# Kernel tuning notes

Measured on AMD Instinct MI355X. Metric: run time of the kernel, lower is better.

Reference implementation:

```python
import jax, jax.numpy as jnp
import numpy as np

L, HID, NH, DH, OUT = 20, 512, 8, 64, 1000
NPAT, PS = 14, 16
IN_DIM = 3 * PS * PS          # 768
SEQ = NPAT * NPAT + 1         # 197
BATCH = 64
EPS = 1e-5


def _pos_embeddings(seq_len, d):
    # sin(i/10000^(j/d)) for even j, cos(i/10000^((j-1)/d)) for odd j
    i = jnp.arange(seq_len, dtype=jnp.float32)[:, None]
    j = jnp.arange(d)
    je = (j - (j % 2)).astype(jnp.float32)
    ang = i / jnp.power(10000.0, je / d)
    return jnp.where(j % 2 == 0, jnp.sin(ang), jnp.cos(ang))


def _layernorm(x, g, b):
    m = jnp.mean(x, axis=-1, keepdims=True)
    v = jnp.mean(jnp.square(x - m), axis=-1, keepdims=True)
    return (x - m) * jax.lax.rsqrt(v + EPS) * g + b


def setup_inputs() -> dict:
    key = jax.random.key(0)
    ks = jax.random.split(key, 12)
    r = lambda k, sh: jax.random.normal(k, sh, dtype=jnp.float32) * 0.02
    return {
        "x": jax.random.normal(ks[0], (BATCH, 3, 224, 224), dtype=jnp.float32),
        "embed_W": r(ks[1], (IN_DIM, HID)),
        "embed_b": jnp.zeros((HID,), jnp.float32),
        "cls": r(ks[2], (HID,)),
        "ln1_g": jnp.ones((L, HID), jnp.float32),
        "ln1_b": jnp.zeros((L, HID), jnp.float32),
        "qW": r(ks[3], (L, NH, DH, DH)),
        "qb": jnp.zeros((L, NH, DH), jnp.float32),
        "kW": r(ks[4], (L, NH, DH, DH)),
        "kb": jnp.zeros((L, NH, DH), jnp.float32),
        "vW": r(ks[5], (L, NH, DH, DH)),
        "vb": jnp.zeros((L, NH, DH), jnp.float32),
        "ln2_g": jnp.ones((L, HID), jnp.float32),
        "ln2_b": jnp.zeros((L, HID), jnp.float32),
        "mlp1_W": r(ks[6], (L, HID, 4 * HID)),
        "mlp1_b": jnp.zeros((L, 4 * HID), jnp.float32),
        "mlp2_W": r(ks[7], (L, 4 * HID, HID)),
        "mlp2_b": jnp.zeros((L, HID), jnp.float32),
        "head_W": r(ks[8], (HID, OUT)),
        "head_b": jnp.zeros((OUT,), jnp.float32),
    }


def reference(x, embed_W, embed_b, cls, ln1_g, ln1_b, qW, qb, kW, kb, vW, vb,
              ln2_g, ln2_b, mlp1_W, mlp1_b, mlp2_W, mlp2_b, head_W, head_b):
    n = x.shape[0]
    # patchify: [n,3,224,224] -> [n,196,768], flatten order (c, ph, pw)
    p = x.reshape(n, 3, NPAT, PS, NPAT, PS)
    p = p.transpose(0, 2, 4, 1, 3, 5).reshape(n, NPAT * NPAT, IN_DIM)
    tokens = p @ embed_W + embed_b                      # [n,196,HID]
    cls_tok = jnp.broadcast_to(cls, (n, 1, HID))
    h = jnp.concatenate([cls_tok, tokens], axis=1)      # [n,197,HID]
    h = h + _pos_embeddings(SEQ, HID)

    scale = 1.0 / jnp.sqrt(jnp.float32(DH))

    def step(h, params):
        (g1, b1, qw, qb_, kw, kb_, vw, vb_, g2, b2, w1, b1m, w2, b2m) = params
        y = _layernorm(h, g1, b1)                       # [n,S,HID]
        yh = y.reshape(n, SEQ, NH, DH)
        # torch Linear: out = seq @ W.T + b; qw stored as [NH, out, in]
        q = jnp.einsum('nshd,hed->nshe', yh, qw) + qb_
        k = jnp.einsum('nshd,hed->nshe', yh, kw) + kb_
        v = jnp.einsum('nshd,hed->nshe', yh, vw) + vb_
        att = jax.nn.softmax(jnp.einsum('nqhd,nkhd->nhqk', q, k) * scale, axis=-1)
        o = jnp.einsum('nhqk,nkhd->nqhd', att, v).reshape(n, SEQ, HID)
        h = h + o
        z = _layernorm(h, g2, b2)
        z = jax.nn.gelu(z @ w1 + b1m, approximate=False) @ w2 + b2m
        return h + z, None

    params = (ln1_g, ln1_b, qW, qb, kW, kb, vW, vb,
              ln2_g, ln2_b, mlp1_W, mlp1_b, mlp2_W, mlp2_b)
    h, _ = jax.lax.scan(step, h, params)
    logits = h[:, 0] @ head_W + head_b
    return jax.nn.softmax(logits, axis=-1)
```

## Files before the change

### kernel.cpp

```cpp
#include <hip/hip_runtime.h>
#include <hip/hip_bf16.h>
#include <math.h>

#define LAY 20
#define HID 512
#define NH 8
#define DH 64
#define OUTC 1000
#define SEQ 197
#define SPAD 224
#define BATCH 64
#define TT (BATCH*SEQ)
#define M2 12800
#define NPTOK (BATCH*196)
#define IN_DIM 768

typedef __attribute__((ext_vector_type(8))) short bf16x8;
typedef __attribute__((ext_vector_type(4))) float f32x4;

__device__ __forceinline__ ushort f2bf(float f){
  __hip_bfloat16 h = __float2bfloat16(f);
  return *(ushort*)&h;
}
__device__ __forceinline__ float bf2f(ushort u){
  __hip_bfloat16 h = *(__hip_bfloat16*)&u;
  return __bfloat162float(h);
}

__device__ __forceinline__ float posemb(int i, int j){
  float je = (float)(j & ~1);
  float ang = (float)i * powf(10000.0f, -je * (1.0f/(float)HID));
  return (j & 1) ? cosf(ang) : sinf(ang);
}

__device__ __forceinline__ float gelu_exact(float x){
  return 0.5f * x * (1.0f + erff(x * 0.70710678118654752f));
}

__device__ __forceinline__ void gld_lds16(const ushort* g, ushort* l){
  __builtin_amdgcn_global_load_lds((const __attribute__((address_space(1))) void*)g,
                                   (__attribute__((address_space(3))) void*)l, 16, 0, 0);
}

__global__ __launch_bounds__(512)
void pos_kernel(float* __restrict__ pos){
  int i = blockIdx.x, j = threadIdx.x;
  pos[(size_t)i*HID + j] = posemb(i, j);
}

__global__ __launch_bounds__(256)
void convt_kernel(const float* __restrict__ src, ushort* __restrict__ dst,
                  int R, int C){
  __shared__ float tile[32][33];
  const float* s = src + (size_t)blockIdx.z * R * C;
  ushort* d      = dst + (size_t)blockIdx.z * R * C;
  int r0 = blockIdx.y * 32, c0 = blockIdx.x * 32;
  int tc = threadIdx.x & 31, tr = threadIdx.x >> 5;
  #pragma unroll
  for (int i = 0; i < 4; ++i)
    tile[tr + i*8][tc] = s[(size_t)(r0 + tr + i*8)*C + c0 + tc];
  __syncthreads();
  #pragma unroll
  for (int i = 0; i < 4; ++i)
    d[(size_t)(c0 + tr + i*8)*R + r0 + tc] = f2bf(tile[tc][tr + i*8]);
}

__global__ __launch_bounds__(256)
void cvt_kernel(const float* __restrict__ src, ushort* __restrict__ dst, int count){
  int idx = blockIdx.x * 256 + threadIdx.x;
  if (idx < count) dst[idx] = f2bf(src[idx]);
}

__global__ __launch_bounds__(256)
void patchify_kernel(const float* __restrict__ x, ushort* __restrict__ p){
  int idx = blockIdx.x * 256 + threadIdx.x;
  int r   = idx / 768, cdx = idx - r * 768;
  int n   = r / 196,  pp  = r - n * 196;
  int pr  = pp / 14,  pc  = pp - pr * 14;
  int c   = cdx >> 8, rem = cdx & 255;
  int ph  = rem >> 4, pw  = rem & 15;
  p[idx] = f2bf(x[ (((size_t)(n*3 + c)*224) + pr*16 + ph)*224 + pc*16 + pw ]);
}

__global__ __launch_bounds__(512)
void cls_kernel(const float* __restrict__ cls, const float* __restrict__ pos,
                float* __restrict__ h){
  int n = blockIdx.x, e = threadIdx.x;
  h[(size_t)n*SEQ*HID + e] = cls[e] + pos[e];
}

template<int BN, int EPI>
__global__ __launch_bounds__(256, 4)
void gemm_pipe(const ushort* __restrict__ A, const ushort* __restrict__ Bt,
               const float* __restrict__ bias, void* __restrict__ Cv,
               int K, int N, int Mreal, int NBX, const float* __restrict__ pos){
  constexpr int BM = 128;
  constexpr int MF = 4, NF = BN/32;
  constexpr int BQ = BN/64;
  constexpr int TBS = 8192 + BN*64;
  constexpr int ES = NF*16 + 12;
  __shared__ char lds[2*TBS];

  int t = threadIdx.x, lane = t & 63, wave = t >> 6;
  int wr = wave >> 1, wn = wave & 1;
  int l16 = lane & 15, g = lane >> 4;

  int NB = gridDim.x;
  int q8 = NB >> 3, r8 = NB & 7;
  int xcd = blockIdx.x & 7, i8 = blockIdx.x >> 3;
  int swz = (xcd < r8 ? xcd*(q8+1) : r8*(q8+1) + (xcd-r8)*q8) + i8;
  int rb = (swz / NBX) * BM, cb = (swz % NBX) * BN;

  const int srow = t >> 2;
  const int kel  = ((t & 3) ^ ((srow >> 1) & 3)) * 8;
  const ushort* pA[2]; const ushort* pB[BQ];
  #pragma unroll
  for (int q = 0; q < 2; ++q)
    pA[q] = A + (size_t)(rb + q*64 + srow)*K + kel;
  #pragma unroll
  for (int q = 0; q < BQ; ++q)
    pB[q] = Bt + (size_t)(cb + q*64 + srow)*K + kel;
  const int sdst = t*16;

  const int sx = (l16 >> 1) & 3;
  int aoff[MF], boff[NF];
  #pragma unroll
  for (int mf = 0; mf < MF; ++mf)
    aoff[mf] = (wr*64 + mf*16 + l16)*64 + ((g ^ sx) << 4);
  #pragma unroll
  for (int nf = 0; nf < NF; ++nf)
    boff[nf] = 8192 + (wn*(NF*16) + nf*16 + l16)*64 + ((g ^ sx) << 4);

  f32x4 acc[MF][NF];
  #pragma unroll
  for (int mf = 0; mf < MF; ++mf)
    #pragma unroll
    for (int nf = 0; nf < NF; ++nf)
      acc[mf][nf] = (f32x4){0.f,0.f,0.f,0.f};

  #pragma unroll
  for (int q = 0; q < 2; ++q)
    gld_lds16(pA[q], (ushort*)(lds + q*4096 + sdst));
  #pragma unroll
  for (int q = 0; q < BQ; ++q)
    gld_lds16(pB[q], (ushort*)(lds + 8192 + q*4096 + sdst));

  int NT = K / 32;
  for (int tt = 0; tt < NT; ++tt){
    const char* cur = lds + (tt & 1)*TBS;
    char* nxt = lds + ((tt & 1) ^ 1)*TBS;
    bool pf = (tt + 1 < NT);
    if (pf){
      const size_t kb = (size_t)(tt + 1) * 32;
      #pragma unroll
      for (int q = 0; q < 2; ++q)
        gld_lds16(pA[q] + kb, (ushort*)(nxt + q*4096 + sdst));
      #pragma unroll
      for (int q = 0; q < BQ; ++q)
        gld_lds16(pB[q] + kb, (ushort*)(nxt + 8192 + q*4096 + sdst));
      if constexpr (BQ == 2)
        asm volatile("s_waitcnt vmcnt(4)" ::: "memory");
      else
        asm volatile("s_waitcnt vmcnt(3)" ::: "memory");
    } else {
      asm volatile("s_waitcnt vmcnt(0)" ::: "memory");
    }
    __builtin_amdgcn_s_barrier();

    bf16x8 af[MF], bfr[NF];
    #pragma unroll
    for (int nf = 0; nf < NF; ++nf)
      bfr[nf] = *(const bf16x8*)(cur + boff[nf]);
    #pragma unroll
    for (int mf = 0; mf < MF; ++mf)
      af[mf] = *(const bf16x8*)(cur + aoff[mf]);

    __builtin_amdgcn_s_setprio(1);
    #pragma unroll
    for (int mf = 0; mf < MF; ++mf)
      #pragma unroll
      for (int nf = 0; nf < NF; ++nf)
        acc[mf][nf] = __builtin_amdgcn_mfma_f32_16x16x32_bf16(af[mf], bfr[nf], acc[mf][nf], 0, 0, 0);
    __builtin_amdgcn_s_setprio(0);
    __builtin_amdgcn_s_barrier();
  }

  float bvv[NF];
  #pragma unroll
  for (int nf = 0; nf < NF; ++nf)
    bvv[nf] = bias[cb + wn*(NF*16) + nf*16 + l16];
  float* eps = (float*)(lds + wave*(16*ES*4));

  #pragma unroll
  for (int mf = 0; mf < MF; ++mf){
    #pragma unroll
    for (int nf = 0; nf < NF; ++nf)
      #pragma unroll
      for (int j = 0; j < 4; ++j){
        float val = acc[mf][nf][j] + bvv[nf];
        if (EPI == 1) val = gelu_exact(val);
        eps[(g*4+j)*ES + nf*16 + l16] = val;
      }
    #pragma unroll
    for (int i = 0; i < NF; ++i){
      int id = i*64 + lane;
      int r = id / (4*NF), c4 = id % (4*NF);
      float4 vv = *(float4*)&eps[r*ES + c4*4];
      int grow = rb + wr*64 + mf*16 + r;
      int gcol = cb + wn*(NF*16) + c4*4;
      if (EPI == 1){
        ushort4 u;
        u.x = f2bf(vv.x); u.y = f2bf(vv.y); u.z = f2bf(vv.z); u.w = f2bf(vv.w);
        *(ushort4*)&((ushort*)Cv)[(size_t)grow*N + gcol] = u;
      } else if (EPI == 2){
        if (grow < Mreal){
          float* cp = &((float*)Cv)[(size_t)grow*N + gcol];
          float4 o = *(float4*)cp;
          o.x += vv.x; o.y += vv.y; o.z += vv.z; o.w += vv.w;
          *(float4*)cp = o;
        }
      } else {
        if (grow < Mreal){
          int bn = grow / 196, sp = grow - bn*196;
          float4 pv = *(const float4*)&pos[(size_t)(1+sp)*HID + gcol];
          vv.x += pv.x; vv.y += pv.y; vv.z += pv.z; vv.w += pv.w;
          *(float4*)&((float*)Cv)[((size_t)bn*SEQ + 1 + sp)*HID + gcol] = vv;
        }
      }
    }
  }
}

__global__ __launch_bounds__(256)
void ln_kernel(const float* __restrict__ x, const float* __restrict__ g,
               const float* __restrict__ b, ushort* __restrict__ y){
  int tok = blockIdx.x, t = threadIdx.x;
  const float* xp = x + (size_t)tok*HID;
  float v1 = xp[t], v2 = xp[t + 256];
  __shared__ float red[4];
  float s = v1 + v2;
  #pragma unroll
  for (int off = 32; off; off >>= 1) s += __shfl_xor(s, off);
  if ((t & 63) == 0) red[t >> 6] = s;
  __syncthreads();
  float mean = (red[0] + red[1] + red[2] + red[3]) * (1.0f/512.0f);
  __syncthreads();
  float d1 = v1 - mean, d2 = v2 - mean;
  s = d1*d1 + d2*d2;
  #pragma unroll
  for (int off = 32; off; off >>= 1) s += __shfl_xor(s, off);
  if ((t & 63) == 0) red[t >> 6] = s;
  __syncthreads();
  float var = (red[0] + red[1] + red[2] + red[3]) * (1.0f/512.0f);
  float rs  = rsqrtf(var + 1e-5f);
  ushort* yp = y + (size_t)tok*HID;
  yp[t]       = f2bf(d1*rs*g[t]       + b[t]);
  yp[t + 256] = f2bf(d2*rs*g[t + 256] + b[t + 256]);
}

__global__ __launch_bounds__(256)
void qkv_mfma(const ushort* __restrict__ y,
              const ushort* __restrict__ wqb, const ushort* __restrict__ wkb,
              const ushort* __restrict__ wvb,
              const float* __restrict__ bq, const float* __restrict__ bk,
              const float* __restrict__ bv,
              ushort* __restrict__ q, ushort* __restrict__ k,
              ushort* __restrict__ v){
  __shared__ short As[128*64];
  __shared__ short Bs[64*64];
  int t = threadIdx.x;
  int lane = t & 63, wave = t >> 6;
  int l16 = lane & 15, g = lane >> 4;
  int p  = blockIdx.y >> 3, hh = blockIdx.y & 7;
  int rb = blockIdx.x * 128;

  const ushort* W; const float* bias; ushort* out;
  if (p == 0)      { W = wqb; bias = bq; out = q; }
  else if (p == 1) { W = wkb; bias = bk; out = k; }
  else             { W = wvb; bias = bv; out = v; }
  W    += (size_t)hh * 64 * 64;
  bias += hh * 64;

  int srow = t >> 3, skoff = (t & 7) * 8;
  const ushort* Ab = y + (size_t)(rb + srow)*HID + hh*64 + skoff;
  const ushort* Bb = W + (size_t)srow*64 + skoff;
  #pragma unroll
  for (int i = 0; i < 4; ++i)
    gld_lds16(Ab + (size_t)(i*32)*HID, (ushort*)&As[t*8 + i*2048]);
  #pragma unroll
  for (int i = 0; i < 2; ++i)
    gld_lds16(Bb + (size_t)(i*32)*64, (ushort*)&Bs[t*8 + i*2048]);
  __syncthreads();

  f32x4 acc[2][4];
  #pragma unroll
  for (int m = 0; m < 2; ++m)
    #pragma unroll
    for (int n = 0; n < 4; ++n)
      acc[m][n] = (f32x4){0.f,0.f,0.f,0.f};

  #pragma unroll
  for (int kc = 0; kc < 2; ++kc){
    bf16x8 af[2], bfr[4];
    #pragma unroll
    for (int m = 0; m < 2; ++m)
      af[m] = *(bf16x8*)&As[(wave*32 + m*16 + l16)*64 + kc*32 + g*8];
    #pragma unroll
    for (int n = 0; n < 4; ++n)
      bfr[n] = *(bf16x8*)&Bs[(n*16 + l16)*64 + kc*32 + g*8];
    #pragma unroll
    for (int m = 0; m < 2; ++m)
      #pragma unroll
      for (int n = 0; n < 4; ++n)
        acc[m][n] = __builtin_amdgcn_mfma_f32_16x16x32_bf16(af[m], bfr[n], acc[m][n], 0, 0, 0);
  }
  __syncthreads();

  float bvv[4];
  #pragma unroll
  for (int nd = 0; nd < 4; ++nd) bvv[nd] = bias[nd*16 + l16];
  ushort* eps = (ushort*)As + wave*(16*72);
  #pragma unroll
  for (int mch = 0; mch < 2; ++mch){
    #pragma unroll
    for (int nd = 0; nd < 4; ++nd)
      #pragma unroll
      for (int j = 0; j < 4; ++j)
        eps[(g*4+j)*72 + nd*16 + l16] = f2bf(acc[mch][nd][j] + bvv[nd]);
    #pragma unroll
    for (int i = 0; i < 2; ++i){
      int id = i*64 + lane;
      int r = id >> 3, c8 = id & 7;
      uint4 vv = *(uint4*)&eps[r*72 + c8*8];
      int tok = rb + wave*32 + mch*16 + r;
      if (tok < TT)
        *(uint4*)&out[(size_t)tok*HID + hh*64 + c8*8] = vv;
    }
  }
}

__global__ __launch_bounds__(512, 4)
void attn_kernel(const ushort* __restrict__ q, const ushort* __restrict__ k,
                 const ushort* __restrict__ v, float* __restrict__ h){
  __shared__ ushort Ks[SPAD*64];
  __shared__ ushort Vs[64*256];
  __shared__ ushort Ps[8][32*40];
  int nh = blockIdx.x;
  int n = nh >> 3, hd = nh & 7;
  int t = threadIdx.x;
  int lane = t & 63, wave = t >> 6;
  int l16 = lane & 15, g = lane >> 4;

  const ushort* kbase = k + ((size_t)n*SEQ)*HID + hd*64;
  for (int c = t; c < 224*8; c += 512){
    int s = c >> 3, c8 = (c & 7) * 8;
    int sr = s < SEQ ? s : SEQ-1;
    uint4 val = *(const uint4*)&kbase[(size_t)sr*HID + c8];
    int byte = s*128 + c8*2;
    byte ^= (s & 7) << 4;
    *(uint4*)((char*)Ks + byte) = val;
  }
  const ushort* vbase = v + ((size_t)n*SEQ)*HID + hd*64;
  for (int c = t; c < 224*8; c += 512){
    int s = c >> 3, d8 = (c & 7) * 8;
    uint4 val = {0u,0u,0u,0u};
    if (s < SEQ) val = *(const uint4*)&vbase[(size_t)s*HID + d8];
    ushort* vsp = (ushort*)Vs;
    #pragma unroll
    for (int e = 0; e < 8; ++e){
      int d = d8 + e;
      int swzi = ((d & 7) ^ ((d >> 3) & 7)) << 4;
      int byte = d*512 + ((s*2) ^ swzi);
      vsp[byte >> 1] = ((ushort*)&val)[e];
    }
  }

  int qrow0 = wave * 32;
  bool wactive = qrow0 < SEQ;
  bf16x8 aq[2][2];
  if (wactive){
    #pragma unroll
    for (int m = 0; m < 2; ++m){
      int row = qrow0 + m*16 + l16;
      int sr = row < SEQ ? row : SEQ-1;
      const ushort* qp = q + ((size_t)n*SEQ + sr)*HID + hd*64;
      #pragma unroll
      for (int kc = 0; kc < 2; ++kc)
        aq[m][kc] = *(const bf16x8*)&qp[kc*32 + g*8];
    }
  }
  __syncthreads();

  if (wactive){
    ushort* myP = &Ps[wave][0];
    f32x4 accO[2][4];
    float mrun[2][4], lrun[2][4];
    #pragma unroll
    for (int m = 0; m < 2; ++m){
      #pragma unroll
      for (int nd = 0; nd < 4; ++nd) accO[m][nd] = (f32x4){0.f,0.f,0.f,0.f};
      #pragma unroll
      for (int j = 0; j < 4; ++j){ mrun[m][j] = -1e30f; lrun[m][j] = 0.f; }
    }

    for (int kt = 0; kt < 7; ++kt){
      f32x4 accS[2][2];
      #pragma unroll
      for (int m = 0; m < 2; ++m)
        #pragma unroll
        for (int nn = 0; nn < 2; ++nn) accS[m][nn] = (f32x4){0.f,0.f,0.f,0.f};
      #pragma unroll
      for (int kc = 0; kc < 2; ++kc){
        bf16x8 bk[2];
        #pragma unroll
        for (int nn = 0; nn < 2; ++nn){
          int srow = kt*32 + nn*16 + l16;
          int byte = srow*128 + kc*64 + g*16;
          byte ^= (srow & 7) << 4;
          bk[nn] = *(const bf16x8*)((const char*)Ks + byte);
        }
        #pragma unroll
        for (int m = 0; m < 2; ++m)
          #pragma unroll
          for (int nn = 0; nn < 2; ++nn)
            accS[m][nn] = __builtin_amdgcn_mfma_f32_16x16x32_bf16(aq[m][kc], bk[nn], accS[m][nn], 0, 0, 0);
      }
      bool kv0 = (kt*32 + l16) < SEQ;
      bool kv1 = (kt*32 + 16 + l16) < SEQ;
      #pragma unroll
      for (int m = 0; m < 2; ++m){
        #pragma unroll
        for (int j = 0; j < 4; ++j){
          float s0 = kv0 ? accS[m][0][j]*0.125f : -1e30f;
          float s1 = kv1 ? accS[m][1][j]*0.125f : -1e30f;
          float mx = fmaxf(s0, s1);
          mx = fmaxf(mx, __shfl_xor(mx, 1));
          mx = fmaxf(mx, __shfl_xor(mx, 2));
          mx = fmaxf(mx, __shfl_xor(mx, 4));
          mx = fmaxf(mx, __shfl_xor(mx, 8));
          float mold = mrun[m][j];
          float mnew = fmaxf(mold, mx);
          float corr = __expf(mold - mnew);
          mrun[m][j] = mnew;
          float p0 = __expf(s0 - mnew);
          float p1 = __expf(s1 - mnew);
          float rs = p0 + p1;
          rs += __shfl_xor(rs, 1);
          rs += __shfl_xor(rs, 2);
          rs += __shfl_xor(rs, 4);
          rs += __shfl_xor(rs, 8);
          lrun[m][j] = lrun[m][j]*corr + rs;
          #pragma unroll
          for (int nd = 0; nd < 4; ++nd) accO[m][nd][j] *= corr;
          int prow = m*16 + g*4 + j;
          myP[prow*40 + l16]      = f2bf(p0);
          myP[prow*40 + 16 + l16] = f2bf(p1);
        }
      }
      bf16x8 ap[2], bv[4];
      #pragma unroll
      for (int m = 0; m < 2; ++m)
        ap[m] = *(const bf16x8*)&myP[(m*16 + l16)*40 + g*8];
      #pragma unroll
      for (int nd = 0; nd < 4; ++nd){
        int d = nd*16 + l16;
        int byte = d*512 + kt*64 + g*16;
        byte ^= ((d & 7) ^ ((d >> 3) & 7)) << 4;
        bv[nd] = *(const bf16x8*)((const char*)Vs + byte);
      }
      #pragma unroll
      for (int m = 0; m < 2; ++m)
        #pragma unroll
        for (int nd = 0; nd < 4; ++nd)
          accO[m][nd] = __builtin_amdgcn_mfma_f32_16x16x32_bf16(ap[m], bv[nd], accO[m][nd], 0, 0, 0);
    }

    #pragma unroll
    for (int m = 0; m < 2; ++m){
      #pragma unroll
      for (int j = 0; j < 4; ++j){
        int row = qrow0 + m*16 + g*4 + j;
        if (row < SEQ){
          float inv = 1.0f / lrun[m][j];
          float* hp = h + ((size_t)n*SEQ + row)*HID + hd*64;
          #pragma unroll
          for (int nd = 0; nd < 4; ++nd)
            hp[nd*16 + l16] += accO[m][nd][j] * inv;
        }
      }
    }
  }
}

__global__ __launch_bounds__(256)
void head_logits(const float* __restrict__ h, const float* __restrict__ W,
                 const float* __restrict__ b, float* __restrict__ logits){
  int c0 = blockIdx.x * 8;
  __shared__ float Ws[512*8];
  int t = threadIdx.x;
  for (int i = t; i < 512*8; i += 256){
    int kx = i >> 3, c = i & 7;
    Ws[i] = W[(size_t)kx*OUTC + c0 + c];
  }
  __syncthreads();
  int n = t >> 2, g = t & 3;
  const float* hp = h + (size_t)n*SEQ*HID + g*128;
  float acc[8] = {};
  for (int kx = 0; kx < 128; ++kx){
    float hv = hp[kx];
    const float* wsr = &Ws[(g*128 + kx)*8];
    #pragma unroll
    for (int c = 0; c < 8; ++c) acc[c] += hv * wsr[c];
  }
  #pragma unroll
  for (int c = 0; c < 8; ++c){
    acc[c] += __shfl_xor(acc[c], 1);
    acc[c] += __shfl_xor(acc[c], 2);
  }
  if (g == 0){
    #pragma unroll
    for (int c = 0; c < 8; ++c)
      logits[(size_t)n*OUTC + c0 + c] = acc[c] + b[c0 + c];
  }
}

__global__ __launch_bounds__(256)
void head_softmax(const float* __restrict__ logits, float* __restrict__ out){
  int n = blockIdx.x, t = threadIdx.x;
  __shared__ float red[4];
  float v[4];
  #pragma unroll
  for (int j = 0; j < 4; ++j){
    int e = t + j*256;
    v[j] = (e < OUTC) ? logits[(size_t)n*OUTC + e] : -1e30f;
  }
  float mx = fmaxf(fmaxf(v[0], v[1]), fmaxf(v[2], v[3]));
  #pragma unroll
  for (int off = 32; off; off >>= 1) mx = fmaxf(mx, __shfl_xor(mx, off));
  if ((t & 63) == 0) red[t >> 6] = mx;
  __syncthreads();
  mx = fmaxf(fmaxf(red[0], red[1]), fmaxf(red[2], red[3]));
  __syncthreads();
  float sum = 0.f;
  #pragma unroll
  for (int j = 0; j < 4; ++j){ v[j] = __expf(v[j] - mx); sum += v[j]; }
  #pragma unroll
  for (int off = 32; off; off >>= 1) sum += __shfl_xor(sum, off);
  if ((t & 63) == 0) red[t >> 6] = sum;
  __syncthreads();
  sum = red[0] + red[1] + red[2] + red[3];
  float inv = 1.0f / sum;
  #pragma unroll
  for (int j = 0; j < 4; ++j){
    int e = t + j*256;
    if (e < OUTC) out[(size_t)n*OUTC + e] = v[j] * inv;
  }
}

extern "C" void kernel_launch(void* const* d_in, const int* in_sizes, int n_in,
                              void* d_out, int out_size, void* d_ws, size_t ws_size,
                              hipStream_t stream){
  const float* x       = (const float*)d_in[0];
  const float* embed_W = (const float*)d_in[1];
  const float* embed_b = (const float*)d_in[2];
  const float* cls     = (const float*)d_in[3];
  const float* ln1_g   = (const float*)d_in[4];
  const float* ln1_b   = (const float*)d_in[5];
  const float* qW      = (const float*)d_in[6];
  const float* qb      = (const float*)d_in[7];
  const float* kW      = (const float*)d_in[8];
  const float* kb      = (const float*)d_in[9];
  const float* vW      = (const float*)d_in[10];
  const float* vb      = (const float*)d_in[11];
  const float* ln2_g   = (const float*)d_in[12];
  const float* ln2_b   = (const float*)d_in[13];
  const float* mlp1_W  = (const float*)d_in[14];
  const float* mlp1_b  = (const float*)d_in[15];
  const float* mlp2_W  = (const float*)d_in[16];
  const float* mlp2_b  = (const float*)d_in[17];
  const float* head_W  = (const float*)d_in[18];
  const float* head_b  = (const float*)d_in[19];
  float* out = (float*)d_out;

  char* wsb = (char*)d_ws;
  float*  h   = (float*)wsb;
  ushort* y   = (ushort*)(wsb + (size_t)M2*HID*4);
  float*  logits = (float*)y;
  char*   un  = wsb + (size_t)M2*HID*4 + (size_t)M2*HID*2;
  ushort* qb_  = (ushort*)un;
  ushort* kb_  = qb_ + (size_t)TT*HID;
  ushort* vb_  = kb_ + (size_t)TT*HID;
  ushort* z1  = (ushort*)un;
  ushort* p   = (ushort*)un;
  char*   wts = un + (size_t)3*TT*HID*4;
  ushort* w1t = (ushort*)wts;
  ushort* w2t = w1t + (size_t)LAY*2048*512;
  ushort* wet = w2t + (size_t)LAY*2048*512;
  ushort* wqb = wet + (size_t)IN_DIM*HID;
  ushort* wkb = wqb + (size_t)LAY*NH*DH*DH;
  ushort* wvb = wkb + (size_t)LAY*NH*DH*DH;
  float*  pos = (float*)(wvb + (size_t)LAY*NH*DH*DH);

  pos_kernel<<<SEQ, 512, 0, stream>>>(pos);
  convt_kernel<<<dim3(2048/32, 512/32, LAY), 256, 0, stream>>>(mlp1_W, w1t, 512, 2048);
  convt_kernel<<<dim3(512/32, 2048/32, LAY), 256, 0, stream>>>(mlp2_W, w2t, 2048, 512);
  convt_kernel<<<dim3(512/32, 768/32, 1),    256, 0, stream>>>(embed_W, wet, 768, 512);
  {
    int cnt = LAY*NH*DH*DH;
    int grd = (cnt + 255)/256;
    cvt_kernel<<<grd, 256, 0, stream>>>(qW, wqb, cnt);
    cvt_kernel<<<grd, 256, 0, stream>>>(kW, wkb, cnt);
    cvt_kernel<<<grd, 256, 0, stream>>>(vW, wvb, cnt);
  }

  patchify_kernel<<<(NPTOK*IN_DIM)/256, 256, 0, stream>>>(x, p);
  cls_kernel<<<BATCH, 512, 0, stream>>>(cls, pos, h);
  gemm_pipe<128, 3><<<(512/128)*(M2/128), 256, 0, stream>>>(
      p, wet, embed_b, h, IN_DIM, HID, NPTOK, 512/128, pos);

  for (int l = 0; l < LAY; ++l){
    ln_kernel<<<TT, 256, 0, stream>>>(h, ln1_g + l*HID, ln1_b + l*HID, y);
    qkv_mfma<<<dim3(M2/128, 24), 256, 0, stream>>>(
        y,
        wqb + (size_t)l*NH*DH*DH, wkb + (size_t)l*NH*DH*DH, wvb + (size_t)l*NH*DH*DH,
        qb + (size_t)l*HID, kb + (size_t)l*HID, vb + (size_t)l*HID,
        qb_, kb_, vb_);
    attn_kernel<<<BATCH*NH, 512, 0, stream>>>(qb_, kb_, vb_, h);
    ln_kernel<<<TT, 256, 0, stream>>>(h, ln2_g + l*HID, ln2_b + l*HID, y);
    gemm_pipe<128, 1><<<(2048/128)*(M2/128), 256, 0, stream>>>(
        y, w1t + (size_t)l*2048*512, mlp1_b + (size_t)l*4*HID, z1,
        HID, 4*HID, TT, 2048/128, pos);
    gemm_pipe<64, 2><<<(512/64)*(M2/128), 256, 0, stream>>>(
        z1, w2t + (size_t)l*2048*512, mlp2_b + (size_t)l*HID, h,
        4*HID, HID, TT, 512/64, pos);
  }

  head_logits<<<125, 256, 0, stream>>>(h, head_W, head_b, logits);
  head_softmax<<<BATCH, 256, 0, stream>>>(logits, out);
}
```

Baseline: 3.612 ms.

## Vectorize layernorm, fuse Q/K/V per block, widen MLP2 tile

Layernorm now runs 128 threads per token and uses float4 loads and stores, so each token needs fewer threads and fewer memory instructions. The QKV kernel computes Q, K and V in one block per head, loading the activation tile once and reusing it from registers against three weight tiles, instead of launching three times as many blocks that each reload it. The second MLP GEMM switches from 64-wide to 128-wide column tiles, which halves its grid and increases reuse per block. The costs are fewer blocks to fill the GPU in QKV and MLP2, plus more shared memory and registers per QKV block.

```diff
diff --git a/kernel.cpp b/kernel.cpp
--- a/kernel.cpp
+++ b/kernel.cpp
@@ -231,31 +231,36 @@
   }
 }
 
-__global__ __launch_bounds__(256)
+__global__ __launch_bounds__(128)
 void ln_kernel(const float* __restrict__ x, const float* __restrict__ g,
                const float* __restrict__ b, ushort* __restrict__ y){
   int tok = blockIdx.x, t = threadIdx.x;
-  const float* xp = x + (size_t)tok*HID;
-  float v1 = xp[t], v2 = xp[t + 256];
-  __shared__ float red[4];
-  float s = v1 + v2;
+  int wave = t >> 6;
+  __shared__ float red[2];
+  float4 v = *(const float4*)&x[(size_t)tok*HID + t*4];
+  float s = (v.x + v.y) + (v.z + v.w);
   #pragma unroll
   for (int off = 32; off; off >>= 1) s += __shfl_xor(s, off);
-  if ((t & 63) == 0) red[t >> 6] = s;
-  __syncthreads();
-  float mean = (red[0] + red[1] + red[2] + red[3]) * (1.0f/512.0f);
-  __syncthreads();
-  float d1 = v1 - mean, d2 = v2 - mean;
-  s = d1*d1 + d2*d2;
+  if ((t & 63) == 0) red[wave] = s;
+  __syncthreads();
+  float mean = (red[0] + red[1]) * (1.0f/512.0f);
+  __syncthreads();
+  float dx = v.x - mean, dy = v.y - mean, dz = v.z - mean, dw = v.w - mean;
+  s = (dx*dx + dy*dy) + (dz*dz + dw*dw);
   #pragma unroll
   for (int off = 32; off; off >>= 1) s += __shfl_xor(s, off);
-  if ((t & 63) == 0) red[t >> 6] = s;
-  __syncthreads();
-  float var = (red[0] + red[1] + red[2] + red[3]) * (1.0f/512.0f);
+  if ((t & 63) == 0) red[wave] = s;
+  __syncthreads();
+  float var = (red[0] + red[1]) * (1.0f/512.0f);
   float rs  = rsqrtf(var + 1e-5f);
-  ushort* yp = y + (size_t)tok*HID;
-  yp[t]       = f2bf(d1*rs*g[t]       + b[t]);
-  yp[t + 256] = f2bf(d2*rs*g[t + 256] + b[t + 256]);
+  float4 gv = *(const float4*)&g[t*4];
+  float4 bv = *(const float4*)&b[t*4];
+  ushort4 o;
+  o.x = f2bf(dx*rs*gv.x + bv.x);
+  o.y = f2bf(dy*rs*gv.y + bv.y);
+  o.z = f2bf(dz*rs*gv.z + bv.z);
+  o.w = f2bf(dw*rs*gv.w + bv.w);
+  *(ushort4*)&y[(size_t)tok*HID + t*4] = o;
 }
 
 __global__ __launch_bounds__(256)
@@ -267,74 +272,80 @@
               ushort* __restrict__ q, ushort* __restrict__ k,
               ushort* __restrict__ v){
   __shared__ short As[128*64];
-  __shared__ short Bs[64*64];
+  __shared__ short Bs[3][64*64];
   int t = threadIdx.x;
   int lane = t & 63, wave = t >> 6;
   int l16 = lane & 15, g = lane >> 4;
-  int p  = blockIdx.y >> 3, hh = blockIdx.y & 7;
+  int hh = blockIdx.y;
   int rb = blockIdx.x * 128;
 
-  const ushort* W; const float* bias; ushort* out;
-  if (p == 0)      { W = wqb; bias = bq; out = q; }
-  else if (p == 1) { W = wkb; bias = bk; out = k; }
-  else             { W = wvb; bias = bv; out = v; }
-  W    += (size_t)hh * 64 * 64;
-  bias += hh * 64;
+  const ushort* Wp[3] = { wqb + (size_t)hh*64*64, wkb + (size_t)hh*64*64, wvb + (size_t)hh*64*64 };
+  const float* biasp[3] = { bq + hh*64, bk + hh*64, bv + hh*64 };
+  ushort* outp[3] = { q, k, v };
 
   int srow = t >> 3, skoff = (t & 7) * 8;
   const ushort* Ab = y + (size_t)(rb + srow)*HID + hh*64 + skoff;
-  const ushort* Bb = W + (size_t)srow*64 + skoff;
   #pragma unroll
   for (int i = 0; i < 4; ++i)
     gld_lds16(Ab + (size_t)(i*32)*HID, (ushort*)&As[t*8 + i*2048]);
   #pragma unroll
-  for (int i = 0; i < 2; ++i)
-    gld_lds16(Bb + (size_t)(i*32)*64, (ushort*)&Bs[t*8 + i*2048]);
-  __syncthreads();
-
-  f32x4 acc[2][4];
-  #pragma unroll
-  for (int m = 0; m < 2; ++m)
-    #pragma unroll
-    for (int n = 0; n < 4; ++n)
-      acc[m][n] = (f32x4){0.f,0.f,0.f,0.f};
-
-  #pragma unroll
-  for (int kc = 0; kc < 2; ++kc){
-    bf16x8 af[2], bfr[4];
+  for (int p = 0; p < 3; ++p){
+    const ushort* Bb = Wp[p] + (size_t)srow*64 + skoff;
+    #pragma unroll
+    for (int i = 0; i < 2; ++i)
+      gld_lds16(Bb + (size_t)(i*32)*64, (ushort*)&Bs[p][t*8 + i*2048]);
+  }
+  __syncthreads();
+
+  bf16x8 af[2][2];
+  #pragma unroll
+  for (int kc = 0; kc < 2; ++kc)
     #pragma unroll
     for (int m = 0; m < 2; ++m)
-      af[m] = *(bf16x8*)&As[(wave*32 + m*16 + l16)*64 + kc*32 + g*8];
-    #pragma unroll
-    for (int n = 0; n < 4; ++n)
-      bfr[n] = *(bf16x8*)&Bs[(n*16 + l16)*64 + kc*32 + g*8];
+      af[kc][m] = *(bf16x8*)&As[(wave*32 + m*16 + l16)*64 + kc*32 + g*8];
+  __syncthreads();
+
+  ushort* eps = (ushort*)As + wave*(16*72);
+  #pragma unroll
+  for (int p = 0; p < 3; ++p){
+    f32x4 acc[2][4];
     #pragma unroll
     for (int m = 0; m < 2; ++m)
       #pragma unroll
       for (int n = 0; n < 4; ++n)
-        acc[m][n] = __builtin_amdgcn_mfma_f32_16x16x32_bf16(af[m], bfr[n], acc[m][n], 0, 0, 0);
-  }
-  __syncthreads();
-
-  float bvv[4];
-  #pragma unroll
-  for (int nd = 0; nd < 4; ++nd) bvv[nd] = bias[nd*16 + l16];
-  ushort* eps = (ushort*)As + wave*(16*72);
-  #pragma unroll
-  for (int mch = 0; mch < 2; ++mch){
-    #pragma unroll
-    for (int nd = 0; nd < 4; ++nd)
-      #pragma unroll
-      for (int j = 0; j < 4; ++j)
-        eps[(g*4+j)*72 + nd*16 + l16] = f2bf(acc[mch][nd][j] + bvv[nd]);
-    #pragma unroll
-    for (int i = 0; i < 2; ++i){
-      int id = i*64 + lane;
-      int r = id >> 3, c8 = id & 7;
-      uint4 vv = *(uint4*)&eps[r*72 + c8*8];
-      int tok = rb + wave*32 + mch*16 + r;
-      if (tok < TT)
-        *(uint4*)&out[(size_t)tok*HID + hh*64 + c8*8] = vv;
+        acc[m][n] = (f32x4){0.f,0.f,0.f,0.f};
+    #pragma unroll
+    for (int kc = 0; kc < 2; ++kc){
+      bf16x8 bfr[4];
+      #pragma unroll
+      for (int n = 0; n < 4; ++n)
+        bfr[n] = *(bf16x8*)&Bs[p][(n*16 + l16)*64 + kc*32 + g*8];
+      #pragma unroll
+      for (int m = 0; m < 2; ++m)
+        #pragma unroll
+        for (int n = 0; n < 4; ++n)
+          acc[m][n] = __builtin_amdgcn_mfma_f32_16x16x32_bf16(af[kc][m], bfr[n], acc[m][n], 0, 0, 0);
+    }
+    float bvv[4];
+    #pragma unroll
+    for (int nd = 0; nd < 4; ++nd) bvv[nd] = biasp[p][nd*16 + l16];
+    ushort* out = outp[p];
+    #pragma unroll
+    for (int mch = 0; mch < 2; ++mch){
+      #pragma unroll
+      for (int nd = 0; nd < 4; ++nd)
+        #pragma unroll
+        for (int j = 0; j < 4; ++j)
+          eps[(g*4+j)*72 + nd*16 + l16] = f2bf(acc[mch][nd][j] + bvv[nd]);
+      #pragma unroll
+      for (int i = 0; i < 2; ++i){
+        int id = i*64 + lane;
+        int r = id >> 3, c8 = id & 7;
+        uint4 vv = *(uint4*)&eps[r*72 + c8*8];
+        int tok = rb + wave*32 + mch*16 + r;
+        if (tok < TT)
+          *(uint4*)&out[(size_t)tok*HID + hh*64 + c8*8] = vv;
+      }
     }
   }
 }
@@ -619,20 +630,20 @@
       p, wet, embed_b, h, IN_DIM, HID, NPTOK, 512/128, pos);
 
   for (int l = 0; l < LAY; ++l){
-    ln_kernel<<<TT, 256, 0, stream>>>(h, ln1_g + l*HID, ln1_b + l*HID, y);
-    qkv_mfma<<<dim3(M2/128, 24), 256, 0, stream>>>(
+    ln_kernel<<<TT, 128, 0, stream>>>(h, ln1_g + l*HID, ln1_b + l*HID, y);
+    qkv_mfma<<<dim3(M2/128, 8), 256, 0, stream>>>(
         y,
         wqb + (size_t)l*NH*DH*DH, wkb + (size_t)l*NH*DH*DH, wvb + (size_t)l*NH*DH*DH,
         qb + (size_t)l*HID, kb + (size_t)l*HID, vb + (size_t)l*HID,
         qb_, kb_, vb_);
     attn_kernel<<<BATCH*NH, 512, 0, stream>>>(qb_, kb_, vb_, h);
-    ln_kernel<<<TT, 256, 0, stream>>>(h, ln2_g + l*HID, ln2_b + l*HID, y);
+    ln_kernel<<<TT, 128, 0, stream>>>(h, ln2_g + l*HID, ln2_b + l*HID, y);
     gemm_pipe<128, 1><<<(2048/128)*(M2/128), 256, 0, stream>>>(
         y, w1t + (size_t)l*2048*512, mlp1_b + (size_t)l*4*HID, z1,
         HID, 4*HID, TT, 2048/128, pos);
-    gemm_pipe<64, 2><<<(512/64)*(M2/128), 256, 0, stream>>>(
+    gemm_pipe<128, 2><<<(512/128)*(M2/128), 256, 0, stream>>>(
         z1, w2t + (size_t)l*2048*512, mlp2_b + (size_t)l*HID, h,
-        4*HID, HID, TT, 512/64, pos);
+        4*HID, HID, TT, 512/128, pos);
   }
 
   head_logits<<<125, 256, 0, stream>>>(h, head_W, head_b, logits);
```

New measurement: 3.170 ms. 12.2% less time.
